# Kernel optimization log

Measured on AMD Instinct MI355X. Metric: run time of the kernel, lower is better.

## Reference

```python
import jax, jax.numpy as jnp
import numpy as np
from jax.ops import segment_sum, segment_max

B, NPG, EPG = 2048, 32, 64          # graphs per drug, nodes/graph, edges/graph
N, E = B * NPG, B * EPG
FIN, EIN = 70, 6
HID, H, C = 128, 2, 64              # hidd_dim, conv heads, head_out_feats
NBLK, NCLASS = 4, 2
CAH, CAD = 8, 128                   # co-attention heads, dim_head


def _elu(x):
    return jnp.where(x > 0, x, jnp.expm1(x))


def _ln_graph(x, batch, w, b):
    # PyG LayerNorm(mode='graph'): normalize over all nodes+channels of each graph.
    cnt = jnp.float32(NPG * x.shape[1])  # all graphs have NPG nodes
    mean = segment_sum(x.sum(-1), batch, num_segments=B) / cnt
    xc = x - mean[batch][:, None]
    var = segment_sum((xc * xc).sum(-1), batch, num_segments=B) / cnt
    return xc * jax.lax.rsqrt(var + 1e-5)[batch][:, None] * w + b


def _ln(x, w, b):
    mu = x.mean(-1, keepdims=True)
    v = ((x - mu) ** 2).mean(-1, keepdims=True)
    return (x - mu) * jax.lax.rsqrt(v + 1e-5) * w + b


def _tconv(x, src, dst, ea, Wq, bq, Wk, bk, Wv, bv, We, Ws, bs):
    # PyG TransformerConv: edge-attention gather -> softmax over incoming edges -> scatter.
    q = (x @ Wq + bq).reshape(-1, H, C)
    k = (x @ Wk + bk).reshape(-1, H, C)
    v = (x @ Wv + bv).reshape(-1, H, C)
    e = (ea @ We).reshape(-1, H, C)
    kj = k[src] + e                                   # [E,H,C]
    a = (q[dst] * kj).sum(-1) * (C ** -0.5)           # [E,H]
    amax = segment_max(a, dst, num_segments=N)
    a = jnp.exp(a - amax[dst])
    a = a / (segment_sum(a, dst, num_segments=N)[dst] + 1e-16)
    out = segment_sum((v[src] + e) * a[:, :, None], dst, num_segments=N)
    return out.reshape(-1, H * C) + x @ Ws + bs       # root/skip connection


def _pool(x, src, dst, ea, batch, ebatch, w_rel, b_rel, w_root, W_re, b_re):
    # SAGPooling(min_score=-1): GraphConv score, per-graph softmax, all nodes kept,
    # then score-weighted global_add_pool; edge_attr pooled per graph and merged.
    agg = segment_sum(x[src], dst, num_segments=N)    # GraphConv 'add' aggregation
    score = agg @ w_rel + b_rel + x @ w_root          # [N]
    smax = segment_max(score, batch, num_segments=B)
    sexp = jnp.exp(score - smax[batch])
    score = sexp / (segment_sum(sexp, batch, num_segments=B)[batch] + 1e-16)
    g = segment_sum(x * score[:, None], batch, num_segments=B)      # [B,HID]
    ge = _elu(segment_sum(ea, ebatch, num_segments=B) @ W_re + b_re)
    g = g * ge
    return g / jnp.maximum(jnp.linalg.norm(g, axis=1, keepdims=True), 1e-12)


def _coattn(qx, kvx, lw, lb, Wq, Wkv, Wo):
    qx = _ln(qx, lw, lb)
    kvx = _ln(kvx, lw, lb)
    b, n = qx.shape[0], qx.shape[1]
    q = (qx @ Wq).reshape(b, n, CAH, CAD).transpose(0, 2, 1, 3)
    k, v = jnp.split(kvx @ Wkv, 2, axis=-1)
    k = k.reshape(b, n, CAH, CAD).transpose(0, 2, 1, 3)
    v = v.reshape(b, n, CAH, CAD).transpose(0, 2, 1, 3)
    attn = jax.nn.softmax(jnp.einsum('bhnd,bhmd->bhnm', q, k) * (CAD ** -0.5), axis=-1)
    o = jnp.einsum('bhnm,bhmd->bhnd', attn, v).transpose(0, 2, 1, 3).reshape(b, n, CAH * CAD)
    return o @ Wo


def setup_inputs() -> dict:
    key = jax.random.key(0)
    ks = iter(jax.random.split(key, 64))

    def nrm(shape, fan):
        return jax.random.normal(next(ks), shape, jnp.float32) * (fan ** -0.5)

    inp = {}
    inp['x1'] = jax.random.normal(next(ks), (N, FIN), jnp.float32)
    inp['x2'] = jax.random.normal(next(ks), (N, FIN), jnp.float32)
    inp['ea1'] = jax.random.normal(next(ks), (E, EIN), jnp.float32)
    inp['ea2'] = jax.random.normal(next(ks), (E, EIN), jnp.float32)
    inp['W_node'] = nrm((FIN, HID), FIN); inp['b_node'] = jnp.zeros((HID,), jnp.float32)
    inp['W_edge'] = nrm((EIN, 64), EIN); inp['b_edge'] = jnp.zeros((64,), jnp.float32)
    inp['ln0_w'] = jnp.ones((HID,), jnp.float32); inp['ln0_b'] = jnp.zeros((HID,), jnp.float32)
    inp['Wq'] = nrm((NBLK, 2, HID, HID), HID); inp['bq'] = jnp.zeros((NBLK, 2, HID), jnp.float32)
    inp['Wk'] = nrm((NBLK, 2, HID, HID), HID); inp['bk'] = jnp.zeros((NBLK, 2, HID), jnp.float32)
    inp['Wv'] = nrm((NBLK, 2, HID, HID), HID); inp['bv'] = jnp.zeros((NBLK, 2, HID), jnp.float32)
    inp['We'] = nrm((NBLK, 2, 64, HID), 64)
    inp['Ws'] = nrm((NBLK, 2, HID, HID), HID); inp['bs'] = jnp.zeros((NBLK, 2, HID), jnp.float32)
    inp['Wup'] = nrm((NBLK, 2, 64, 64), 64); inp['bup'] = jnp.zeros((NBLK, 2, 64), jnp.float32)
    inp['lnw'] = jnp.ones((NBLK, 2, HID), jnp.float32); inp['lnb'] = jnp.zeros((NBLK, 2, HID), jnp.float32)
    inp['w_rel'] = nrm((HID,), HID); inp['b_rel'] = jnp.zeros((), jnp.float32)
    inp['w_root'] = nrm((HID,), HID)
    inp['W_re'] = nrm((64, HID), 64); inp['b_re'] = jnp.zeros((HID,), jnp.float32)
    inp['ca_lw'] = jnp.ones((HID,), jnp.float32); inp['ca_lb'] = jnp.zeros((HID,), jnp.float32)
    inp['Wq_ca'] = nrm((HID, CAH * CAD), HID)
    inp['Wkv_ca'] = nrm((HID, 2 * CAH * CAD), HID)
    inp['Wo_ca'] = nrm((CAH * CAD, HID), CAH * CAD)
    inp['W_merge'] = nrm((NBLK * NBLK, NCLASS), NBLK * NBLK)
    inp['b_merge'] = jnp.zeros((NCLASS,), jnp.float32)
    off = jnp.repeat(jnp.arange(B, dtype=jnp.int32) * NPG, EPG)
    inp['edge_index1'] = jax.random.randint(next(ks), (2, E), 0, NPG, jnp.int32) + off[None, :]
    inp['edge_index2'] = jax.random.randint(next(ks), (2, E), 0, NPG, jnp.int32) + off[None, :]
    inp['batch1'] = jnp.repeat(jnp.arange(B, dtype=jnp.int32), NPG)
    inp['batch2'] = jnp.repeat(jnp.arange(B, dtype=jnp.int32), NPG)
    inp['ebatch1'] = jnp.repeat(jnp.arange(B, dtype=jnp.int32), EPG)
    inp['ebatch2'] = jnp.repeat(jnp.arange(B, dtype=jnp.int32), EPG)
    return inp


def reference(x1, x2, ea1, ea2, W_node, b_node, W_edge, b_edge, ln0_w, ln0_b,
              Wq, bq, Wk, bk, Wv, bv, We, Ws, bs, Wup, bup, lnw, lnb,
              w_rel, b_rel, w_root, W_re, b_re, ca_lw, ca_lb, Wq_ca, Wkv_ca, Wo_ca,
              W_merge, b_merge, edge_index1, edge_index2, batch1, batch2, ebatch1, ebatch2):
    s1, d1 = edge_index1[0], edge_index1[1]
    s2, d2 = edge_index2[0], edge_index2[1]
    x1 = _elu(_ln_graph(x1 @ W_node + b_node, batch1, ln0_w, ln0_b))
    x2 = _elu(_ln_graph(x2 @ W_node + b_node, batch2, ln0_w, ln0_b))
    ea1 = _elu(ea1 @ W_edge + b_edge)
    ea2 = _elu(ea2 @ W_edge + b_edge)

    def block(i, x, ea, src, dst, batch):
        x = _tconv(x, src, dst, ea, Wq[i, 0], bq[i, 0], Wk[i, 0], bk[i, 0],
                   Wv[i, 0], bv[i, 0], We[i, 0], Ws[i, 0], bs[i, 0])
        x = _elu(_ln_graph(x, batch, lnw[i, 0], lnb[i, 0]))
        ea = _elu(ea @ Wup[i, 0] + bup[i, 0])
        x = _tconv(x, src, dst, ea, Wq[i, 1], bq[i, 1], Wk[i, 1], bk[i, 1],
                   Wv[i, 1], bv[i, 1], We[i, 1], Ws[i, 1], bs[i, 1])
        ea_next = ea @ Wup[i, 1] + bup[i, 1]
        x = _elu(_ln_graph(x, batch, lnw[i, 1], lnb[i, 1]))
        return x, _elu(ea_next)

    hs, ts = [], []
    for i in range(NBLK):
        x1, ea1 = block(i, x1, ea1, s1, d1, batch1)
        x2, ea2 = block(i, x2, ea2, s2, d2, batch2)
        hs.append(_pool(x1, s1, d1, ea1, batch1, ebatch1, w_rel, b_rel, w_root, W_re, b_re))
        ts.append(_pool(x2, s2, d2, ea2, batch2, ebatch2, w_rel, b_rel, w_root, W_re, b_re))
    rh = jnp.stack(hs, 1)  # [B, NBLK, HID]
    rt = jnp.stack(ts, 1)
    ha = _coattn(rh, rt, ca_lw, ca_lb, Wq_ca, Wkv_ca, Wo_ca)
    ta = _coattn(rt, rh, ca_lw, ca_lb, Wq_ca, Wkv_ca, Wo_ca)
    m = jnp.einsum('bnd,bmd->bnm', ha, ta).reshape(ha.shape[0], NBLK * NBLK)
    return jax.nn.softmax(m @ W_merge + b_merge, axis=-1)
```

## Files before the change

### kernel.cpp

```cpp
#include <hip/hip_runtime.h>
#include <cstddef>
#include <cstdint>

#define NGRAPH 2048
#define NPG    32
#define EPG    64
#define NNODE  (NGRAPH*NPG)
#define NEDGE  (NGRAPH*EPG)
#define FINDIM 70
#define EINDIM 6
#define HID    128
#define NBLK   4
#define CAH    8
#define CAD    128
#define ES     68
#define XS     132

typedef __attribute__((ext_vector_type(8))) short bf16x8_t;
typedef __attribute__((ext_vector_type(4))) float f32x4;
typedef unsigned short ushortb;

#define MF3(accv, Ah_, Al_, Bh_, Bl_)                                          \
  accv = __builtin_amdgcn_mfma_f32_16x16x32_bf16(Ah_, Bh_, accv, 0, 0, 0);     \
  accv = __builtin_amdgcn_mfma_f32_16x16x32_bf16(Ah_, Bl_, accv, 0, 0, 0);     \
  accv = __builtin_amdgcn_mfma_f32_16x16x32_bf16(Al_, Bh_, accv, 0, 0, 0);

__device__ inline void split8(const float* p, bf16x8_t& h, bf16x8_t& l) {
  float4 v0 = *(const float4*)p, v1 = *(const float4*)(p + 4);
  float vv[8] = {v0.x, v0.y, v0.z, v0.w, v1.x, v1.y, v1.z, v1.w};
#pragma unroll
  for (int j = 0; j < 8; j++) {
    unsigned u = __builtin_bit_cast(unsigned, vv[j]);
    h[j] = (short)(u >> 16);
    float r = vv[j] - __builtin_bit_cast(float, u & 0xFFFF0000u);
    l[j] = (short)(__builtin_bit_cast(unsigned, r) >> 16);
  }
}

template<bool BIAS, bool ELU>
__global__ __launch_bounds__(256) void gemm_kernel(
    const float* __restrict__ A, const float* __restrict__ W,
    const float* __restrict__ bias, float* __restrict__ C,
    int M, int K, int Nc) {
  __shared__ float As[8][64];
  __shared__ float Bs[8][65];
  const int bm = blockIdx.y * 64, bn = blockIdx.x * 64;
  const int tid = threadIdx.x;
  const int tr = tid >> 4, tc = tid & 15;
  float acc[4][4];
#pragma unroll
  for (int i = 0; i < 4; i++)
#pragma unroll
    for (int j = 0; j < 4; j++) acc[i][j] = 0.f;
  for (int k0 = 0; k0 < K; k0 += 8) {
#pragma unroll
    for (int l = 0; l < 2; l++) {
      int idx = tid + l * 256;
      int r = idx >> 3, c = idx & 7;
      As[c][r] = (k0 + c < K) ? A[(size_t)(bm + r) * K + k0 + c] : 0.f;
      int rw = idx >> 6, cw = idx & 63;
      Bs[rw][cw] = (k0 + rw < K) ? W[(size_t)(k0 + rw) * Nc + bn + cw] : 0.f;
    }
    __syncthreads();
#pragma unroll
    for (int kk = 0; kk < 8; kk++) {
      float a_[4], w_[4];
#pragma unroll
      for (int i = 0; i < 4; i++) a_[i] = As[kk][tr * 4 + i];
#pragma unroll
      for (int j = 0; j < 4; j++) w_[j] = Bs[kk][tc * 4 + j];
#pragma unroll
      for (int i = 0; i < 4; i++)
#pragma unroll
        for (int j = 0; j < 4; j++) acc[i][j] += a_[i] * w_[j];
    }
    __syncthreads();
  }
#pragma unroll
  for (int i = 0; i < 4; i++) {
    int r = bm + tr * 4 + i;
#pragma unroll
    for (int j = 0; j < 4; j++) {
      int c = bn + tc * 4 + j;
      float v = acc[i][j];
      if (BIAS) v += bias[c];
      if (ELU) v = v > 0.f ? v : expm1f(v);
      C[(size_t)r * Nc + c] = v;
    }
  }
}

static void run_gemm(const float* A, const float* W, const float* bias, float* C,
                     int M, int K, int Nc, bool eluf, hipStream_t st) {
  dim3 grid(Nc / 64, M / 64), block(256);
  if (eluf) gemm_kernel<true, true><<<grid, block, 0, st>>>(A, W, bias, C, M, K, Nc);
  else      gemm_kernel<true, false><<<grid, block, 0, st>>>(A, W, bias, C, M, K, Nc);
}

__global__ void convw_kernel(const float* __restrict__ src, ushortb* __restrict__ h,
                             ushortb* __restrict__ l, int K, int N, int total,
                             int dstN, int nOff) {
  int idx = blockIdx.x * 256 + threadIdx.x;
  if (idx >= total) return;
  int k = idx % K;
  int t2 = idx / K;
  int n = t2 % N;
  int b = t2 / N;
  float v = src[((size_t)b * K + k) * N + n];
  unsigned uv = __builtin_bit_cast(unsigned, v);
  ushortb hb = (ushortb)(uv >> 16);
  float hf = __builtin_bit_cast(float, uv & 0xFFFF0000u);
  float rr = v - hf;
  ushortb lb = (ushortb)(__builtin_bit_cast(unsigned, rr) >> 16);
  size_t didx = ((size_t)b * dstN + nOff + n) * K + k;
  h[didx] = hb;
  l[didx] = lb;
}

__global__ void bcat_kernel(const float* __restrict__ bq, const float* __restrict__ bk,
                            const float* __restrict__ bv, float* __restrict__ o) {
  int t = blockIdx.x * 256 + threadIdx.x;
  if (t >= 8 * 384) return;
  int pi = t / 384, c = t % 384, sel = c >> 7, cc = c & 127;
  const float* s = sel == 0 ? bq : (sel == 1 ? bk : bv);
  o[t] = s[pi * 128 + cc];
}

__global__ __launch_bounds__(512) void gemm_mfma8_kernel(
    const float* __restrict__ A, const ushortb* __restrict__ Wh,
    const ushortb* __restrict__ Wl, float* __restrict__ C, int M, int K, int N) {
  __shared__ ushortb Ah[128 * 40];
  __shared__ ushortb Al[128 * 40];
  const int bm = blockIdx.y * 128, bn = blockIdx.x * 128;
  const int tid = threadIdx.x, lane = tid & 63, w = tid >> 6;
  const int wr = w >> 1, wc = w & 1;
  const int l16 = lane & 15, lk = lane >> 4;
  f32x4 acc[2][4];
#pragma unroll
  for (int m = 0; m < 2; m++)
#pragma unroll
    for (int n = 0; n < 4; n++) acc[m][n] = (f32x4)0.f;

  for (int k0 = 0; k0 < K; k0 += 32) {
    __syncthreads();
#pragma unroll
    for (int p = 0; p < 2; p++) {
      int base = p * 2048 + tid * 4;
      int r = base >> 5, c = base & 31;
      const float4 v = *(const float4*)(A + (size_t)(bm + r) * K + k0 + c);
      unsigned u0 = __builtin_bit_cast(unsigned, v.x);
      unsigned u1 = __builtin_bit_cast(unsigned, v.y);
      unsigned u2 = __builtin_bit_cast(unsigned, v.z);
      unsigned u3 = __builtin_bit_cast(unsigned, v.w);
      ushort4 hv;
      hv.x = (ushortb)(u0 >> 16); hv.y = (ushortb)(u1 >> 16);
      hv.z = (ushortb)(u2 >> 16); hv.w = (ushortb)(u3 >> 16);
      float r0 = v.x - __builtin_bit_cast(float, u0 & 0xFFFF0000u);
      float r1 = v.y - __builtin_bit_cast(float, u1 & 0xFFFF0000u);
      float r2 = v.z - __builtin_bit_cast(float, u2 & 0xFFFF0000u);
      float r3 = v.w - __builtin_bit_cast(float, u3 & 0xFFFF0000u);
      ushort4 lv;
      lv.x = (ushortb)(__builtin_bit_cast(unsigned, r0) >> 16);
      lv.y = (ushortb)(__builtin_bit_cast(unsigned, r1) >> 16);
      lv.z = (ushortb)(__builtin_bit_cast(unsigned, r2) >> 16);
      lv.w = (ushortb)(__builtin_bit_cast(unsigned, r3) >> 16);
      *(ushort4*)(&Ah[r * 40 + c]) = hv;
      *(ushort4*)(&Al[r * 40 + c]) = lv;
    }
    __syncthreads();
    bf16x8_t bh[4], bl[4];
#pragma unroll
    for (int n = 0; n < 4; n++) {
      size_t o = (size_t)(bn + wc * 64 + n * 16 + l16) * K + k0 + lk * 8;
      bh[n] = *(const bf16x8_t*)(Wh + o);
      bl[n] = *(const bf16x8_t*)(Wl + o);
    }
    bf16x8_t ah[2], al2[2];
#pragma unroll
    for (int m = 0; m < 2; m++) {
      int ao = (wr * 32 + m * 16 + l16) * 40 + lk * 8;
      ah[m]  = *(const bf16x8_t*)(&Ah[ao]);
      al2[m] = *(const bf16x8_t*)(&Al[ao]);
    }
#pragma unroll
    for (int m = 0; m < 2; m++)
#pragma unroll
      for (int n = 0; n < 4; n++) {
        MF3(acc[m][n], ah[m], al2[m], bh[n], bl[n]);
      }
  }
#pragma unroll
  for (int m = 0; m < 2; m++)
#pragma unroll
    for (int n = 0; n < 4; n++) {
      int col = bn + wc * 64 + n * 16 + l16;
#pragma unroll
      for (int r = 0; r < 4; r++) {
        int row = bm + wr * 32 + m * 16 + lk * 4 + r;
        C[(size_t)row * N + col] = acc[m][n][r];
      }
    }
}

static void run_mf8(const float* A, const ushortb* Wh, const ushortb* Wl,
                    float* C, int M, int K, int N, hipStream_t st) {
  dim3 grid(N / 128, M / 128), block(512);
  gemm_mfma8_kernel<<<grid, block, 0, st>>>(A, Wh, Wl, C, M, K, N);
}

__global__ void ln_graph_elu_kernel(const float* __restrict__ in, float* __restrict__ out,
                                    const float* __restrict__ w, const float* __restrict__ b) {
  const int g = blockIdx.x, t = threadIdx.x;
  const float* xg = in + (size_t)g * NPG * HID;
  float* og = out + (size_t)g * NPG * HID;
  float vals[16];
  float s = 0.f, ss = 0.f;
#pragma unroll
  for (int i = 0; i < 16; i++) {
    float v = xg[t + i * 256];
    vals[i] = v; s += v; ss += v * v;
  }
  __shared__ float ws0[4], ws1[4];
  for (int off = 32; off > 0; off >>= 1) { s += __shfl_down(s, off); ss += __shfl_down(ss, off); }
  int wid = t >> 6, lane = t & 63;
  if (lane == 0) { ws0[wid] = s; ws1[wid] = ss; }
  __syncthreads();
  if (t == 0) {
    float S = 0.f, SS = 0.f;
    for (int i = 0; i < 4; i++) { S += ws0[i]; SS += ws1[i]; }
    float mean = S / 4096.f;
    float var = SS / 4096.f - mean * mean;
    ws0[0] = mean; ws1[0] = rsqrtf(var + 1e-5f);
  }
  __syncthreads();
  float mean = ws0[0], inv = ws1[0];
#pragma unroll
  for (int i = 0; i < 16; i++) {
    int idx = t + i * 256;
    int ch = idx & 127;
    float y = (vals[i] - mean) * inv * w[ch] + b[ch];
    og[idx] = y > 0.f ? y : expm1f(y);
  }
}

template<bool POOL>
__global__ __launch_bounds__(256, 4) void mega_kernel(
    float* __restrict__ xb, float* __restrict__ ea,
    const ushortb* __restrict__ Wqkvh, const ushortb* __restrict__ Wqkvl,
    const ushortb* __restrict__ Wsh, const ushortb* __restrict__ Wsl,
    const ushortb* __restrict__ WeTh, const ushortb* __restrict__ WeTl,
    const ushortb* __restrict__ Wuph, const ushortb* __restrict__ Wupl,
    const float* __restrict__ bqkv_, const float* __restrict__ bs_,
    const float* __restrict__ bup_, const float* __restrict__ lnw_,
    const float* __restrict__ lnb_,
    const float* __restrict__ w_rel, const float* __restrict__ b_rel,
    const float* __restrict__ w_root, const float* __restrict__ W_re,
    const float* __restrict__ b_re, float* __restrict__ outp, int blk,
    const int* __restrict__ src, const int* __restrict__ dst) {
  const int g = blockIdx.x, t = threadIdx.x;
  const int lane = t & 63, w = t >> 6, l16 = lane & 15, lk = lane >> 4;
  __shared__ float el[EPG * ES];
  __shared__ float qs2[NPG * ES];
  __shared__ float ks2[NPG * ES];
  __shared__ unsigned char lists[NPG * EPG];
  __shared__ int deg_[NPG];
  __shared__ int sl[EPG], dl[EPG];
  __shared__ float alE[128];
  __shared__ float red0[NPG], red1[NPG];

  if (t < EPG) { sl[t] = src[g * EPG + t] - g * NPG; dl[t] = dst[g * EPG + t] - g * NPG; }
  if (t < NPG) {
    int c = 0;
    for (int e = 0; e < EPG; e++)
      if (dl[e] == t) lists[t * EPG + (c++)] = (unsigned char)e;
    deg_[t] = c;
  }

  bf16x8_t xh[2][4], xL[2][4];
#pragma unroll
  for (int m = 0; m < 2; m++)
#pragma unroll
    for (int kc = 0; kc < 4; kc++)
      split8(xb + ((size_t)g * NPG + m * 16 + l16) * HID + kc * 32 + lk * 8,
             xh[m][kc], xL[m][kc]);
  const float* eag = ea + ((size_t)g * EPG + w * 16 + l16) * 64;

  float accH0[8], accH1[8];
#pragma unroll
  for (int c = 0; c < 8; c++) { accH0[c] = 0.f; accH1[c] = 0.f; }

  auto proj = [&](int baseN, float* dstL) {
    f32x4 pa0 = (f32x4)0.f, pa1 = (f32x4)0.f;
#pragma unroll
    for (int kc = 0; kc < 4; kc++) {
      size_t o = (size_t)(baseN + w * 16 + l16) * HID + kc * 32 + lk * 8;
      bf16x8_t bh = *(const bf16x8_t*)(Wqkvh + o);
      bf16x8_t bl = *(const bf16x8_t*)(Wqkvl + o);
      MF3(pa0, xh[0][kc], xL[0][kc], bh, bl);
      MF3(pa1, xh[1][kc], xL[1][kc], bh, bl);
    }
    float bv = bqkv_[baseN + w * 16 + l16];
#pragma unroll
    for (int r = 0; r < 4; r++) {
      dstL[(lk * 4 + r) * ES + w * 16 + l16] = pa0[r] + bv;
      dstL[(16 + lk * 4 + r) * ES + w * 16 + l16] = pa1[r] + bv;
    }
  };

  auto head = [&](const int h, float (&acc8)[8]) {
    {
      bf16x8_t ea0h, ea0l, ea1h, ea1l;
      split8(eag + lk * 8, ea0h, ea0l);
      split8(eag + 32 + lk * 8, ea1h, ea1l);
#pragma unroll 1
      for (int n = 0; n < 4; n++) {
        f32x4 acc = (f32x4)0.f;
        size_t o0 = (size_t)(h * 64 + n * 16 + l16) * 64 + lk * 8;
        bf16x8_t bh0 = *(const bf16x8_t*)(WeTh + o0);
        bf16x8_t bl0 = *(const bf16x8_t*)(WeTl + o0);
        MF3(acc, ea0h, ea0l, bh0, bl0);
        bf16x8_t bh1 = *(const bf16x8_t*)(WeTh + o0 + 32);
        bf16x8_t bl1 = *(const bf16x8_t*)(WeTl + o0 + 32);
        MF3(acc, ea1h, ea1l, bh1, bl1);
#pragma unroll
        for (int r = 0; r < 4; r++)
          el[(w * 16 + lk * 4 + r) * ES + n * 16 + l16] = acc[r];
      }
    }
    proj(h * 64, qs2);
    proj(128 + h * 64, ks2);
    __syncthreads();
    {
      const int e2 = t >> 2, part = t & 3;
      const float* qp = qs2 + dl[e2] * ES + part * 16;
      const float* kp = ks2 + sl[e2] * ES + part * 16;
      const float* ep = el + e2 * ES + part * 16;
      float s = 0.f;
#pragma unroll
      for (int c = 0; c < 16; c += 4) {
        float4 qv = *(const float4*)(qp + c);
        float4 kv = *(const float4*)(kp + c);
        float4 ev = *(const float4*)(ep + c);
        s += qv.x * (kv.x + ev.x) + qv.y * (kv.y + ev.y) +
             qv.z * (kv.z + ev.z) + qv.w * (kv.w + ev.w);
      }
      s += __shfl_xor(s, 1);
      s += __shfl_xor(s, 2);
      if (part == 0) alE[e2] = s * 0.125f;
    }
    __syncthreads();
    {
      const int n = t >> 3, part = t & 7;
      float m = -1e30f;
#pragma unroll 1
      for (int i = 0; i < 8; i++) {
        int e2 = part * 8 + i;
        if (dl[e2] == n) m = fmaxf(m, alE[e2]);
      }
      m = fmaxf(m, __shfl_xor(m, 1));
      m = fmaxf(m, __shfl_xor(m, 2));
      m = fmaxf(m, __shfl_xor(m, 4));
      float su = 0.f;
#pragma unroll 1
      for (int i = 0; i < 8; i++) {
        int e2 = part * 8 + i;
        if (dl[e2] == n) su += expf(alE[e2] - m);
      }
      su += __shfl_xor(su, 1);
      su += __shfl_xor(su, 2);
      su += __shfl_xor(su, 4);
      if (part == 0) { red0[n] = m; red1[n] = su; }
    }
    __syncthreads();
    if (t < EPG) {
      int n = dl[t];
      alE[t] = expf(alE[t] - red0[n]) / (red1[n] + 1e-16f);
    }
    f32x4 va0 = (f32x4)0.f, va1 = (f32x4)0.f;
#pragma unroll
    for (int kc = 0; kc < 4; kc++) {
      size_t o = (size_t)(256 + h * 64 + w * 16 + l16) * HID + kc * 32 + lk * 8;
      bf16x8_t bh = *(const bf16x8_t*)(Wqkvh + o);
      bf16x8_t bl = *(const bf16x8_t*)(Wqkvl + o);
      MF3(va0, xh[0][kc], xL[0][kc], bh, bl);
      MF3(va1, xh[1][kc], xL[1][kc], bh, bl);
    }
    float bv = bqkv_[256 + h * 64 + w * 16 + l16];
    __syncthreads();
#pragma unroll
    for (int r = 0; r < 4; r++) {
      ks2[(lk * 4 + r) * ES + w * 16 + l16] = va0[r] + bv;
      ks2[(16 + lk * 4 + r) * ES + w * 16 + l16] = va1[r] + bv;
    }
    __syncthreads();
    {
      const int n = t >> 3, cg = t & 7;
      const int dg = deg_[n];
      for (int i = 0; i < dg; i++) {
        const int e2 = lists[n * EPG + i];
        const float a = alE[e2];
        const float* vp = ks2 + sl[e2] * ES + cg * 8;
        const float* ep = el + e2 * ES + cg * 8;
        float4 v0 = *(const float4*)vp, v1 = *(const float4*)(vp + 4);
        float4 e0 = *(const float4*)ep, e1 = *(const float4*)(ep + 4);
        acc8[0] += a * (v0.x + e0.x); acc8[1] += a * (v0.y + e0.y);
        acc8[2] += a * (v0.z + e0.z); acc8[3] += a * (v0.w + e0.w);
        acc8[4] += a * (v1.x + e1.x); acc8[5] += a * (v1.y + e1.y);
        acc8[6] += a * (v1.z + e1.z); acc8[7] += a * (v1.w + e1.w);
      }
    }
    __syncthreads();
  };

  head(0, accH0);
  head(1, accH1);

  {
#pragma unroll
    for (int n = 0; n < 2; n++) {
      f32x4 sa0 = (f32x4)0.f, sa1 = (f32x4)0.f;
#pragma unroll
      for (int kc = 0; kc < 4; kc++) {
        size_t o = (size_t)(w * 32 + n * 16 + l16) * HID + kc * 32 + lk * 8;
        bf16x8_t bh = *(const bf16x8_t*)(Wsh + o);
        bf16x8_t bl = *(const bf16x8_t*)(Wsl + o);
        MF3(sa0, xh[0][kc], xL[0][kc], bh, bl);
        MF3(sa1, xh[1][kc], xL[1][kc], bh, bl);
      }
      int col = w * 32 + n * 16 + l16;
      float bv = bs_[col];
#pragma unroll
      for (int r = 0; r < 4; r++) {
        el[(lk * 4 + r) * XS + col] = sa0[r] + bv;
        el[(16 + lk * 4 + r) * XS + col] = sa1[r] + bv;
      }
    }
  }
  f32x4 ua[4];
  {
    bf16x8_t ea0h, ea0l, ea1h, ea1l;
    split8(eag + lk * 8, ea0h, ea0l);
    split8(eag + 32 + lk * 8, ea1h, ea1l);
#pragma unroll
    for (int n = 0; n < 4; n++) {
      f32x4 acc = (f32x4)0.f;
      size_t o0 = (size_t)(n * 16 + l16) * 64 + lk * 8;
      bf16x8_t bh0 = *(const bf16x8_t*)(Wuph + o0);
      bf16x8_t bl0 = *(const bf16x8_t*)(Wupl + o0);
      MF3(acc, ea0h, ea0l, bh0, bl0);
      bf16x8_t bh1 = *(const bf16x8_t*)(Wuph + o0 + 32);
      bf16x8_t bl1 = *(const bf16x8_t*)(Wupl + o0 + 32);
      MF3(acc, ea1h, ea1l, bh1, bl1);
      int col = n * 16 + l16;
      float bv = bup_[col];
#pragma unroll
      for (int r = 0; r < 4; r++) {
        float y = acc[r] + bv;
        y = y > 0.f ? y : expm1f(y);
        ua[n][r] = y;
        ea[((size_t)g * EPG + w * 16 + lk * 4 + r) * 64 + col] = y;
      }
    }
  }
  __syncthreads();
  {
    const int n = t >> 3, cg = t & 7;
    float v16[16];
#pragma unroll
    for (int c = 0; c < 8; c++) {
      v16[c] = accH0[c] + el[n * XS + cg * 8 + c];
      v16[8 + c] = accH1[c] + el[n * XS + 64 + cg * 8 + c];
    }
    float s = 0.f, ss = 0.f;
#pragma unroll
    for (int j = 0; j < 16; j++) { s += v16[j]; ss += v16[j] * v16[j]; }
    for (int o2 = 32; o2 > 0; o2 >>= 1) { s += __shfl_down(s, o2); ss += __shfl_down(ss, o2); }
    if (lane == 0) { red0[w] = s; red1[w] = ss; }
    __syncthreads();
    if (t == 0) {
      float S = red0[0] + red0[1] + red0[2] + red0[3];
      float SS = red1[0] + red1[1] + red1[2] + red1[3];
      float mean = S / 4096.f;
      float var = SS / 4096.f - mean * mean;
      red0[0] = mean; red1[0] = rsqrtf(var + 1e-5f);
    }
    __syncthreads();
    float mean = red0[0], inv = red1[0];
    float* xg = xb + (size_t)g * NPG * HID;
#pragma unroll
    for (int hh = 0; hh < 2; hh++)
#pragma unroll
      for (int c = 0; c < 8; c++) {
        int col = hh * 64 + cg * 8 + c;
        float y = (v16[hh * 8 + c] - mean) * inv * lnw_[col] + lnb_[col];
        y = y > 0.f ? y : expm1f(y);
        xg[n * HID + col] = y;
        el[n * XS + col] = y;
      }
  }

  if constexpr (POOL) {
    __syncthreads();
    {
#pragma unroll
      for (int n = 0; n < 4; n++) {
        float s = ua[n][0] + ua[n][1] + ua[n][2] + ua[n][3];
        s += __shfl_xor(s, 16);
        s += __shfl_xor(s, 32);
        if (lk == 0) qs2[w * 64 + n * 16 + l16] = s;
      }
      const int n = t >> 3, part = t & 7;
      float s = 0.f;
      for (int c = part * 16; c < part * 16 + 16; c++)
        s += el[n * XS + c] * w_root[c];
      const int dg = deg_[n];
      for (int i = 0; i < dg; i++) {
        int sn = sl[lists[n * EPG + i]];
        for (int c = part * 16; c < part * 16 + 16; c++)
          s += el[sn * XS + c] * w_rel[c];
      }
      s += __shfl_xor(s, 1);
      s += __shfl_xor(s, 2);
      s += __shfl_xor(s, 4);
      if (part == 0) alE[n] = s + b_rel[0];
    }
    __syncthreads();
    if (t < 64)
      alE[64 + t] = qs2[t] + qs2[64 + t] + qs2[128 + t] + qs2[192 + t];
    if (t >= 128 && t < 160) {
      int n = t - 128;
      float sc = alE[n];
      float m = sc;
      for (int o2 = 1; o2 <= 16; o2 <<= 1) m = fmaxf(m, __shfl_xor(m, o2));
      float e = expf(sc - m);
      float su = e;
      for (int o2 = 1; o2 <= 16; o2 <<= 1) su += __shfl_xor(su, o2);
      alE[n] = e / (su + 1e-16f);
    }
    __syncthreads();
    if (t < HID) {
      const int ch = t;
      float gv = 0.f;
      for (int n = 0; n < NPG; n++) gv += alE[n] * el[n * XS + ch];
      float s2 = b_re[ch];
      for (int k2 = 0; k2 < 64; k2++) s2 += alE[64 + k2] * W_re[k2 * HID + ch];
      s2 = s2 > 0.f ? s2 : expm1f(s2);
      float gl = gv * s2;
      qs2[256 + ch] = gl;
      float sq = gl * gl;
      for (int o2 = 32; o2 > 0; o2 >>= 1) sq += __shfl_down(sq, o2);
      if (lane == 0) red0[w] = sq;
    }
    __syncthreads();
    if (t == 0) red1[0] = fmaxf(sqrtf(red0[0] + red0[1]), 1e-12f);
    __syncthreads();
    if (t < HID)
      outp[((size_t)g * NBLK + blk) * HID + t] = qs2[256 + t] / red1[0];
  }
}

__global__ void ln_row_kernel(const float* __restrict__ in, float* __restrict__ out,
                              const float* __restrict__ w, const float* __restrict__ b) {
  const int r = blockIdx.x, t = threadIdx.x;
  float v = in[(size_t)r * HID + t];
  float s = v, ss = v * v;
  for (int off = 32; off > 0; off >>= 1) { s += __shfl_down(s, off); ss += __shfl_down(ss, off); }
  __shared__ float s0[2], s1[2];
  if ((t & 63) == 0) { s0[t >> 6] = s; s1[t >> 6] = ss; }
  __syncthreads();
  float S = s0[0] + s0[1], SS = s1[0] + s1[1];
  float mean = S / 128.f, var = SS / 128.f - mean * mean;
  out[(size_t)r * HID + t] = (v - mean) * rsqrtf(var + 1e-5f) * w[t] + b[t];
}

__global__ void coattn_kernel(const float* __restrict__ qb, const float* __restrict__ kvb,
                              float* __restrict__ ob) {
  const int bh = blockIdx.x, b = bh >> 3, h = bh & 7, t = threadIdx.x;
  __shared__ float attn[4][4];
  __shared__ float red[64];
  const int pair = t >> 2, part = t & 3;
  const int n = pair >> 2, m = pair & 3;
  const float* qp = qb + ((size_t)(b * 4 + n) * (CAH * CAD)) + h * CAD;
  const float* kp = kvb + ((size_t)(b * 4 + m) * (2 * CAH * CAD)) + h * CAD;
  float s = 0.f;
  for (int d = part * 32; d < part * 32 + 32; d++) s += qp[d] * kp[d];
  red[t] = s;
  __syncthreads();
  if (t < 16) {
    float sc = (red[t * 4] + red[t * 4 + 1] + red[t * 4 + 2] + red[t * 4 + 3]) * 0.08838834764831845f;
    attn[t >> 2][t & 3] = sc;
  }
  __syncthreads();
  if (t < 4) {
    float m_ = -1e30f;
    for (int j = 0; j < 4; j++) m_ = fmaxf(m_, attn[t][j]);
    float ex[4], su = 0.f;
    for (int j = 0; j < 4; j++) { ex[j] = expf(attn[t][j] - m_); su += ex[j]; }
    for (int j = 0; j < 4; j++) attn[t][j] = ex[j] / su;
  }
  __syncthreads();
  for (int i = t; i < 512; i += 64) {
    int n2 = i >> 7, d = i & 127;
    float acc = 0.f;
    for (int m2 = 0; m2 < 4; m2++)
      acc += attn[n2][m2] * kvb[((size_t)(b * 4 + m2) * (2 * CAH * CAD)) + CAH * CAD + h * CAD + d];
    ob[((size_t)(b * 4 + n2) * (CAH * CAD)) + h * CAD + d] = acc;
  }
}

__global__ void final_kernel(const float* __restrict__ ha, const float* __restrict__ ta,
                             const float* __restrict__ Wm, const float* __restrict__ bm,
                             float* __restrict__ out) {
  const int b = blockIdx.x, t = threadIdx.x;
  __shared__ float mm[16];
  if (t < 16) {
    int n = t >> 2, m2 = t & 3;
    const float* hp = ha + (size_t)(b * 4 + n) * HID;
    const float* tp = ta + (size_t)(b * 4 + m2) * HID;
    float s = 0.f;
    for (int c = 0; c < HID; c++) s += hp[c] * tp[c];
    mm[t] = s;
  }
  __syncthreads();
  if (t == 0) {
    float l0 = bm[0], l1 = bm[1];
    for (int j = 0; j < 16; j++) { l0 += mm[j] * Wm[j * 2]; l1 += mm[j] * Wm[j * 2 + 1]; }
    float m_ = fmaxf(l0, l1);
    float e0 = expf(l0 - m_), e1 = expf(l1 - m_);
    float su = e0 + e1;
    out[b * 2] = e0 / su;
    out[b * 2 + 1] = e1 / su;
  }
}

extern "C" void kernel_launch(void* const* d_in, const int* in_sizes, int n_in,
                              void* d_out, int out_size, void* d_ws, size_t ws_size,
                              hipStream_t stream) {
  const float* xin[2]  = {(const float*)d_in[0], (const float*)d_in[1]};
  const float* eain[2] = {(const float*)d_in[2], (const float*)d_in[3]};
  const float* W_node = (const float*)d_in[4];
  const float* b_node = (const float*)d_in[5];
  const float* W_edge = (const float*)d_in[6];
  const float* b_edge = (const float*)d_in[7];
  const float* ln0_w = (const float*)d_in[8];
  const float* ln0_b = (const float*)d_in[9];
  const float* Wq = (const float*)d_in[10];
  const float* bq = (const float*)d_in[11];
  const float* Wk = (const float*)d_in[12];
  const float* bk = (const float*)d_in[13];
  const float* Wv = (const float*)d_in[14];
  const float* bv = (const float*)d_in[15];
  const float* We = (const float*)d_in[16];
  const float* Wskip = (const float*)d_in[17];
  const float* bs = (const float*)d_in[18];
  const float* Wup = (const float*)d_in[19];
  const float* bup = (const float*)d_in[20];
  const float* lnw = (const float*)d_in[21];
  const float* lnb = (const float*)d_in[22];
  const float* w_rel = (const float*)d_in[23];
  const float* b_rel = (const float*)d_in[24];
  const float* w_root = (const float*)d_in[25];
  const float* W_re = (const float*)d_in[26];
  const float* b_re = (const float*)d_in[27];
  const float* ca_lw = (const float*)d_in[28];
  const float* ca_lb = (const float*)d_in[29];
  const float* Wq_ca = (const float*)d_in[30];
  const float* Wkv_ca = (const float*)d_in[31];
  const float* Wo_ca = (const float*)d_in[32];
  const float* W_merge = (const float*)d_in[33];
  const float* b_merge = (const float*)d_in[34];
  const int* ei[2] = {(const int*)d_in[35], (const int*)d_in[36]};
  float* out = (float*)d_out;
  (void)in_sizes; (void)n_in; (void)out_size;

  char* base = (char*)d_ws;
  size_t off = 0;
  auto alloc = [&](size_t elems) {
    float* r = (float*)(base + off);
    off += ((elems * 4 + 255) & ~(size_t)255);
    return r;
  };
  auto allocb = [&](size_t elems) {
    ushortb* r = (ushortb*)(base + off);
    off += ((elems * 2 + 255) & ~(size_t)255);
    return r;
  };
  float* xb  = alloc((size_t)NNODE * HID);
  float* ea  = alloc((size_t)NEDGE * 64);
  float* big = alloc((size_t)8192 * 2048);
  float* hs  = alloc((size_t)NGRAPH * NBLK * HID);
  float* ts  = alloc((size_t)NGRAPH * NBLK * HID);
  float* rhn = alloc((size_t)NGRAPH * NBLK * HID);
  float* rtn = alloc((size_t)NGRAPH * NBLK * HID);
  float* hab = alloc((size_t)NGRAPH * NBLK * HID);
  float* tab = alloc((size_t)NGRAPH * NBLK * HID);
  ushortb* Wqkvh = allocb((size_t)8 * 384 * 128); ushortb* Wqkvl = allocb((size_t)8 * 384 * 128);
  ushortb* Wsh = allocb(8 * 16384);  ushortb* Wsl = allocb(8 * 16384);
  ushortb* Wuph = allocb(8 * 4096);  ushortb* Wupl = allocb(8 * 4096);
  ushortb* WeTh = allocb(8 * 8192);  ushortb* WeTl = allocb(8 * 8192);
  ushortb* Wqcah = allocb(131072);   ushortb* Wqcal = allocb(131072);
  ushortb* Wkvh = allocb(262144);    ushortb* Wkvl = allocb(262144);
  ushortb* Woh = allocb(131072);     ushortb* Wol = allocb(131072);
  float* bqkv = alloc(8 * 384);
  if (off > ws_size) return;

  float* qc  = xb;
  float* kvc = big;
  float* oc  = ea;

  auto convw = [&](const float* s, ushortb* h, ushortb* l, int K, int N, int B,
                   int dstN, int nOff) {
    int tot = B * K * N;
    convw_kernel<<<(tot + 255) / 256, 256, 0, stream>>>(s, h, l, K, N, tot, dstN, nOff);
  };
  convw(Wq, Wqkvh, Wqkvl, 128, 128, 8, 384, 0);
  convw(Wk, Wqkvh, Wqkvl, 128, 128, 8, 384, 128);
  convw(Wv, Wqkvh, Wqkvl, 128, 128, 8, 384, 256);
  convw(Wskip, Wsh, Wsl, 128, 128, 8, 128, 0);
  convw(Wup, Wuph, Wupl, 64, 64, 8, 64, 0);
  convw(We, WeTh, WeTl, 64, 128, 8, 128, 0);
  convw(Wq_ca, Wqcah, Wqcal, 128, 1024, 1, 1024, 0);
  convw(Wkv_ca, Wkvh, Wkvl, 128, 2048, 1, 2048, 0);
  convw(Wo_ca, Woh, Wol, 1024, 128, 1, 128, 0);
  bcat_kernel<<<(8 * 384 + 255) / 256, 256, 0, stream>>>(bq, bk, bv, bqkv);

  for (int d2 = 0; d2 < 2; ++d2) {
    const int* src = ei[d2];
    const int* dst = ei[d2] + NEDGE;
    run_gemm(xin[d2], W_node, b_node, xb, NNODE, FINDIM, HID, false, stream);
    ln_graph_elu_kernel<<<NGRAPH, 256, 0, stream>>>(xb, xb, ln0_w, ln0_b);
    run_gemm(eain[d2], W_edge, b_edge, ea, NEDGE, EINDIM, 64, true, stream);
    float* outp = d2 == 0 ? hs : ts;
    for (int i = 0; i < NBLK; ++i) {
      int pi0 = i * 2, pi1 = i * 2 + 1;
      mega_kernel<false><<<NGRAPH, 256, 0, stream>>>(
          xb, ea,
          Wqkvh + (size_t)pi0 * 49152, Wqkvl + (size_t)pi0 * 49152,
          Wsh + (size_t)pi0 * 16384, Wsl + (size_t)pi0 * 16384,
          WeTh + (size_t)pi0 * 8192, WeTl + (size_t)pi0 * 8192,
          Wuph + (size_t)pi0 * 4096, Wupl + (size_t)pi0 * 4096,
          bqkv + pi0 * 384, bs + pi0 * 128, bup + pi0 * 64,
          lnw + pi0 * 128, lnb + pi0 * 128,
          w_rel, b_rel, w_root, W_re, b_re, nullptr, 0, src, dst);
      mega_kernel<true><<<NGRAPH, 256, 0, stream>>>(
          xb, ea,
          Wqkvh + (size_t)pi1 * 49152, Wqkvl + (size_t)pi1 * 49152,
          Wsh + (size_t)pi1 * 16384, Wsl + (size_t)pi1 * 16384,
          WeTh + (size_t)pi1 * 8192, WeTl + (size_t)pi1 * 8192,
          Wuph + (size_t)pi1 * 4096, Wupl + (size_t)pi1 * 4096,
          bqkv + pi1 * 384, bs + pi1 * 128, bup + pi1 * 64,
          lnw + pi1 * 128, lnb + pi1 * 128,
          w_rel, b_rel, w_root, W_re, b_re, outp, i, src, dst);
    }
  }

  ln_row_kernel<<<NGRAPH * NBLK, 128, 0, stream>>>(hs, rhn, ca_lw, ca_lb);
  ln_row_kernel<<<NGRAPH * NBLK, 128, 0, stream>>>(ts, rtn, ca_lw, ca_lb);
  run_mf8(rhn, Wqcah, Wqcal, qc, NGRAPH * NBLK, 128, 1024, stream);
  run_mf8(rtn, Wkvh, Wkvl, kvc, NGRAPH * NBLK, 128, 2048, stream);
  coattn_kernel<<<NGRAPH * CAH, 64, 0, stream>>>(qc, kvc, oc);
  run_mf8(oc, Woh, Wol, hab, NGRAPH * NBLK, 1024, 128, stream);
  run_mf8(rtn, Wqcah, Wqcal, qc, NGRAPH * NBLK, 128, 1024, stream);
  run_mf8(rhn, Wkvh, Wkvl, kvc, NGRAPH * NBLK, 128, 2048, stream);
  coattn_kernel<<<NGRAPH * CAH, 64, 0, stream>>>(qc, kvc, oc);
  run_mf8(oc, Woh, Wol, tab, NGRAPH * NBLK, 1024, 128, stream);

  final_kernel<<<NGRAPH, 64, 0, stream>>>(hab, tab, W_merge, b_merge, out);
}
```

Baseline: 3.239 ms.

## Store node and edge activations as pre-split bf16 hi/lo pairs between kernels

Node features and edge attributes are now kept in global memory as separate bf16 high and low halves instead of fp32. The mega kernel loads these directly as MFMA operands, so it no longer re-splits fp32 values on every read. An extra conversion kernel is added for the initial edge embedding, and the pooling scratch moves into a different shared buffer. Total bytes stored stay the same, but stores become scattered ushort writes to two arrays, and the buffer aliasing for the co-attention stage changes.

After: 3.421 ms. +5.6%, slower.

```diff
diff --git a/kernel.cpp b/kernel.cpp
--- a/kernel.cpp
+++ b/kernel.cpp
@@ -25,16 +25,11 @@
   accv = __builtin_amdgcn_mfma_f32_16x16x32_bf16(Ah_, Bl_, accv, 0, 0, 0);     \
   accv = __builtin_amdgcn_mfma_f32_16x16x32_bf16(Al_, Bh_, accv, 0, 0, 0);
 
-__device__ inline void split8(const float* p, bf16x8_t& h, bf16x8_t& l) {
-  float4 v0 = *(const float4*)p, v1 = *(const float4*)(p + 4);
-  float vv[8] = {v0.x, v0.y, v0.z, v0.w, v1.x, v1.y, v1.z, v1.w};
-#pragma unroll
-  for (int j = 0; j < 8; j++) {
-    unsigned u = __builtin_bit_cast(unsigned, vv[j]);
-    h[j] = (short)(u >> 16);
-    float r = vv[j] - __builtin_bit_cast(float, u & 0xFFFF0000u);
-    l[j] = (short)(__builtin_bit_cast(unsigned, r) >> 16);
-  }
+__device__ inline void hl_of(float v, ushortb& h, ushortb& l) {
+  unsigned u = __builtin_bit_cast(unsigned, v);
+  h = (ushortb)(u >> 16);
+  float r = v - __builtin_bit_cast(float, u & 0xFFFF0000u);
+  l = (ushortb)(__builtin_bit_cast(unsigned, r) >> 16);
 }
 
 template<bool BIAS, bool ELU>
@@ -107,14 +102,21 @@
   int n = t2 % N;
   int b = t2 / N;
   float v = src[((size_t)b * K + k) * N + n];
-  unsigned uv = __builtin_bit_cast(unsigned, v);
-  ushortb hb = (ushortb)(uv >> 16);
-  float hf = __builtin_bit_cast(float, uv & 0xFFFF0000u);
-  float rr = v - hf;
-  ushortb lb = (ushortb)(__builtin_bit_cast(unsigned, rr) >> 16);
+  ushortb hb, lb;
+  hl_of(v, hb, lb);
   size_t didx = ((size_t)b * dstN + nOff + n) * K + k;
   h[didx] = hb;
   l[didx] = lb;
+}
+
+__global__ void conv_hl_kernel(const float* __restrict__ in, ushortb* __restrict__ h,
+                               ushortb* __restrict__ l, int total) {
+  int idx = blockIdx.x * 256 + threadIdx.x;
+  if (idx >= total) return;
+  ushortb hb, lb;
+  hl_of(in[idx], hb, lb);
+  h[idx] = hb;
+  l[idx] = lb;
 }
 
 __global__ void bcat_kernel(const float* __restrict__ bq, const float* __restrict__ bk,
@@ -148,22 +150,11 @@
       int base = p * 2048 + tid * 4;
       int r = base >> 5, c = base & 31;
       const float4 v = *(const float4*)(A + (size_t)(bm + r) * K + k0 + c);
-      unsigned u0 = __builtin_bit_cast(unsigned, v.x);
-      unsigned u1 = __builtin_bit_cast(unsigned, v.y);
-      unsigned u2 = __builtin_bit_cast(unsigned, v.z);
-      unsigned u3 = __builtin_bit_cast(unsigned, v.w);
-      ushort4 hv;
-      hv.x = (ushortb)(u0 >> 16); hv.y = (ushortb)(u1 >> 16);
-      hv.z = (ushortb)(u2 >> 16); hv.w = (ushortb)(u3 >> 16);
-      float r0 = v.x - __builtin_bit_cast(float, u0 & 0xFFFF0000u);
-      float r1 = v.y - __builtin_bit_cast(float, u1 & 0xFFFF0000u);
-      float r2 = v.z - __builtin_bit_cast(float, u2 & 0xFFFF0000u);
-      float r3 = v.w - __builtin_bit_cast(float, u3 & 0xFFFF0000u);
-      ushort4 lv;
-      lv.x = (ushortb)(__builtin_bit_cast(unsigned, r0) >> 16);
-      lv.y = (ushortb)(__builtin_bit_cast(unsigned, r1) >> 16);
-      lv.z = (ushortb)(__builtin_bit_cast(unsigned, r2) >> 16);
-      lv.w = (ushortb)(__builtin_bit_cast(unsigned, r3) >> 16);
+      ushort4 hv, lv;
+      hl_of(v.x, hv.x, lv.x);
+      hl_of(v.y, hv.y, lv.y);
+      hl_of(v.z, hv.z, lv.z);
+      hl_of(v.w, hv.w, lv.w);
       *(ushort4*)(&Ah[r * 40 + c]) = hv;
       *(ushort4*)(&Al[r * 40 + c]) = lv;
     }
@@ -208,11 +199,11 @@
   gemm_mfma8_kernel<<<grid, block, 0, st>>>(A, Wh, Wl, C, M, K, N);
 }
 
-__global__ void ln_graph_elu_kernel(const float* __restrict__ in, float* __restrict__ out,
+__global__ void ln_graph_elu_kernel(const float* __restrict__ in,
+                                    ushortb* __restrict__ oh, ushortb* __restrict__ ol,
                                     const float* __restrict__ w, const float* __restrict__ b) {
   const int g = blockIdx.x, t = threadIdx.x;
   const float* xg = in + (size_t)g * NPG * HID;
-  float* og = out + (size_t)g * NPG * HID;
   float vals[16];
   float s = 0.f, ss = 0.f;
 #pragma unroll
@@ -239,13 +230,18 @@
     int idx = t + i * 256;
     int ch = idx & 127;
     float y = (vals[i] - mean) * inv * w[ch] + b[ch];
-    og[idx] = y > 0.f ? y : expm1f(y);
+    y = y > 0.f ? y : expm1f(y);
+    ushortb hb, lb;
+    hl_of(y, hb, lb);
+    oh[(size_t)g * NPG * HID + idx] = hb;
+    ol[(size_t)g * NPG * HID + idx] = lb;
   }
 }
 
 template<bool POOL>
 __global__ __launch_bounds__(256, 4) void mega_kernel(
-    float* __restrict__ xb, float* __restrict__ ea,
+    ushortb* __restrict__ xbh, ushortb* __restrict__ xbl,
+    ushortb* __restrict__ eah, ushortb* __restrict__ eal,
     const ushortb* __restrict__ Wqkvh, const ushortb* __restrict__ Wqkvl,
     const ushortb* __restrict__ Wsh, const ushortb* __restrict__ Wsl,
     const ushortb* __restrict__ WeTh, const ushortb* __restrict__ WeTl,
@@ -276,14 +272,17 @@
     deg_[t] = c;
   }
 
+  const size_t xbase = (size_t)g * NPG * HID;
   bf16x8_t xh[2][4], xL[2][4];
 #pragma unroll
   for (int m = 0; m < 2; m++)
 #pragma unroll
-    for (int kc = 0; kc < 4; kc++)
-      split8(xb + ((size_t)g * NPG + m * 16 + l16) * HID + kc * 32 + lk * 8,
-             xh[m][kc], xL[m][kc]);
-  const float* eag = ea + ((size_t)g * EPG + w * 16 + l16) * 64;
+    for (int kc = 0; kc < 4; kc++) {
+      size_t o = xbase + (size_t)(m * 16 + l16) * HID + kc * 32 + lk * 8;
+      xh[m][kc] = *(const bf16x8_t*)(xbh + o);
+      xL[m][kc] = *(const bf16x8_t*)(xbl + o);
+    }
+  const size_t ebase = ((size_t)g * EPG + w * 16 + l16) * 64 + lk * 8;
 
   float accH0[8], accH1[8];
 #pragma unroll
@@ -309,9 +308,10 @@
 
   auto head = [&](const int h, float (&acc8)[8]) {
     {
-      bf16x8_t ea0h, ea0l, ea1h, ea1l;
-      split8(eag + lk * 8, ea0h, ea0l);
-      split8(eag + 32 + lk * 8, ea1h, ea1l);
+      bf16x8_t ea0h = *(const bf16x8_t*)(eah + ebase);
+      bf16x8_t ea0l = *(const bf16x8_t*)(eal + ebase);
+      bf16x8_t ea1h = *(const bf16x8_t*)(eah + ebase + 32);
+      bf16x8_t ea1l = *(const bf16x8_t*)(eal + ebase + 32);
 #pragma unroll 1
       for (int n = 0; n < 4; n++) {
         f32x4 acc = (f32x4)0.f;
@@ -438,9 +438,10 @@
   }
   f32x4 ua[4];
   {
-    bf16x8_t ea0h, ea0l, ea1h, ea1l;
-    split8(eag + lk * 8, ea0h, ea0l);
-    split8(eag + 32 + lk * 8, ea1h, ea1l);
+    bf16x8_t ea0h = *(const bf16x8_t*)(eah + ebase);
+    bf16x8_t ea0l = *(const bf16x8_t*)(eal + ebase);
+    bf16x8_t ea1h = *(const bf16x8_t*)(eah + ebase + 32);
+    bf16x8_t ea1l = *(const bf16x8_t*)(eal + ebase + 32);
 #pragma unroll
     for (int n = 0; n < 4; n++) {
       f32x4 acc = (f32x4)0.f;
@@ -458,7 +459,11 @@
         float y = acc[r] + bv;
         y = y > 0.f ? y : expm1f(y);
         ua[n][r] = y;
-        ea[((size_t)g * EPG + w * 16 + lk * 4 + r) * 64 + col] = y;
+        ushortb hb, lb;
+        hl_of(y, hb, lb);
+        size_t o = ((size_t)g * EPG + w * 16 + lk * 4 + r) * 64 + col;
+        eah[o] = hb;
+        eal[o] = lb;
       }
     }
   }
@@ -486,7 +491,6 @@
     }
     __syncthreads();
     float mean = red0[0], inv = red1[0];
-    float* xg = xb + (size_t)g * NPG * HID;
 #pragma unroll
     for (int hh = 0; hh < 2; hh++)
 #pragma unroll
@@ -494,7 +498,10 @@
         int col = hh * 64 + cg * 8 + c;
         float y = (v16[hh * 8 + c] - mean) * inv * lnw_[col] + lnb_[col];
         y = y > 0.f ? y : expm1f(y);
-        xg[n * HID + col] = y;
+        ushortb hb, lb;
+        hl_of(y, hb, lb);
+        xbh[xbase + n * HID + col] = hb;
+        xbl[xbase + n * HID + col] = lb;
         el[n * XS + col] = y;
       }
   }
@@ -546,7 +553,7 @@
       for (int k2 = 0; k2 < 64; k2++) s2 += alE[64 + k2] * W_re[k2 * HID + ch];
       s2 = s2 > 0.f ? s2 : expm1f(s2);
       float gl = gv * s2;
-      qs2[256 + ch] = gl;
+      el[4224 + ch] = gl;
       float sq = gl * gl;
       for (int o2 = 32; o2 > 0; o2 >>= 1) sq += __shfl_down(sq, o2);
       if (lane == 0) red0[w] = sq;
@@ -555,7 +562,7 @@
     if (t == 0) red1[0] = fmaxf(sqrtf(red0[0] + red0[1]), 1e-12f);
     __syncthreads();
     if (t < HID)
-      outp[((size_t)g * NBLK + blk) * HID + t] = qs2[256 + t] / red1[0];
+      outp[((size_t)g * NBLK + blk) * HID + t] = el[4224 + t] / red1[0];
   }
 }
 
@@ -685,8 +692,10 @@
     off += ((elems * 2 + 255) & ~(size_t)255);
     return r;
   };
-  float* xb  = alloc((size_t)NNODE * HID);
-  float* ea  = alloc((size_t)NEDGE * 64);
+  ushortb* xbh = allocb((size_t)NNODE * HID);
+  ushortb* xbl = allocb((size_t)NNODE * HID);
+  ushortb* eah = allocb((size_t)NEDGE * 64);
+  ushortb* eal = allocb((size_t)NEDGE * 64);
   float* big = alloc((size_t)8192 * 2048);
   float* hs  = alloc((size_t)NGRAPH * NBLK * HID);
   float* ts  = alloc((size_t)NGRAPH * NBLK * HID);
@@ -704,9 +713,11 @@
   float* bqkv = alloc(8 * 384);
   if (off > ws_size) return;
 
-  float* qc  = xb;
+  float* xtmp = big;
+  float* eatmp = big + (size_t)NNODE * HID;
+  float* qc  = (float*)xbh;
+  float* oc  = (float*)eah;
   float* kvc = big;
-  float* oc  = ea;
 
   auto convw = [&](const float* s, ushortb* h, ushortb* l, int K, int N, int B,
                    int dstN, int nOff) {
@@ -727,14 +738,15 @@
   for (int d2 = 0; d2 < 2; ++d2) {
     const int* src = ei[d2];
     const int* dst = ei[d2] + NEDGE;
-    run_gemm(xin[d2], W_node, b_node, xb, NNODE, FINDIM, HID, false, stream);
-    ln_graph_elu_kernel<<<NGRAPH, 256, 0, stream>>>(xb, xb, ln0_w, ln0_b);
-    run_gemm(eain[d2], W_edge, b_edge, ea, NEDGE, EINDIM, 64, true, stream);
+    run_gemm(xin[d2], W_node, b_node, xtmp, NNODE, FINDIM, HID, false, stream);
+    ln_graph_elu_kernel<<<NGRAPH, 256, 0, stream>>>(xtmp, xbh, xbl, ln0_w, ln0_b);
+    run_gemm(eain[d2], W_edge, b_edge, eatmp, NEDGE, EINDIM, 64, true, stream);
+    conv_hl_kernel<<<(NEDGE * 64 + 255) / 256, 256, 0, stream>>>(eatmp, eah, eal, NEDGE * 64);
     float* outp = d2 == 0 ? hs : ts;
     for (int i = 0; i < NBLK; ++i) {
       int pi0 = i * 2, pi1 = i * 2 + 1;
       mega_kernel<false><<<NGRAPH, 256, 0, stream>>>(
-          xb, ea,
+          xbh, xbl, eah, eal,
           Wqkvh + (size_t)pi0 * 49152, Wqkvl + (size_t)pi0 * 49152,
           Wsh + (size_t)pi0 * 16384, Wsl + (size_t)pi0 * 16384,
           WeTh + (size_t)pi0 * 8192, WeTl + (size_t)pi0 * 8192,
@@ -743,7 +755,7 @@
           lnw + pi0 * 128, lnb + pi0 * 128,
           w_rel, b_rel, w_root, W_re, b_re, nullptr, 0, src, dst);
       mega_kernel<true><<<NGRAPH, 256, 0, stream>>>(
-          xb, ea,
+          xbh, xbl, eah, eal,
           Wqkvh + (size_t)pi1 * 49152, Wqkvl + (size_t)pi1 * 49152,
           Wsh + (size_t)pi1 * 16384, Wsl + (size_t)pi1 * 16384,
           WeTh + (size_t)pi1 * 8192, WeTl + (size_t)pi1 * 8192,
```
